# Kernel optimization log

Hardware: AMD Instinct MI355X
Metric: run time of the kernel (lower is better)

Reference implementation:

```python
import jax, jax.numpy as jnp
import numpy as np

TEMPERATURE = 0.5

def setup_inputs() -> dict:
    key = jax.random.key(0)
    k1, k2 = jax.random.split(key)
    B, D = 4096, 256
    return {
        "first_transformed": jax.random.normal(k1, (B, D), dtype=jnp.float32),
        "second_transformed": jax.random.normal(k2, (B, D), dtype=jnp.float32),
    }

def reference(first_transformed, second_transformed):
    B = first_transformed.shape[0]
    z = jnp.concatenate([first_transformed, second_transformed], axis=0)  # [2B, D]
    z = z / jnp.linalg.norm(z, axis=1, keepdims=True)
    sim = jnp.matmul(z, z.T) / TEMPERATURE  # [2B, 2B]
    n = 2 * B
    # exclude self-similarity from the denominator (mask diagonal)
    diag_mask = jnp.eye(n, dtype=bool)
    denom = jax.nn.logsumexp(jnp.where(diag_mask, -jnp.inf, sim), axis=1)  # [2B]
    # positive pair for row i is row (i+B) mod 2B
    pos_idx = (jnp.arange(n) + B) % n
    pos = sim[jnp.arange(n), pos_idx]  # [2B]
    # loss = 1/(2B) * sum_i (-log(exp(pos_i)/denom_i)) = mean(denom - pos)
    return jnp.mean(denom - pos)
```

## Files before the change

kernel.cpp:

```cpp
#include <hip/hip_runtime.h>
#include <hip/hip_bf16.h>
#include <math.h>


#define NROWS 8192
#define BHALF 4096
#define DDIM  256
#define ROWB  512
#define JSPLIT 16
#define JCHUNK (NROWS / JSPLIT)
#define JT 64
#define NTILES (JCHUNK / JT)
#define TILEB (JT * ROWB)

#define SQRT_K1 1.6986436f
#define LN2F 0.6931471805599453f

typedef __attribute__((ext_vector_type(8))) __bf16 bf16x8;
typedef __attribute__((ext_vector_type(4))) float f32x4;

#if __has_builtin(__builtin_amdgcn_exp2f)
#define FEXP2(x) __builtin_amdgcn_exp2f(x)
#else
#define FEXP2(x) __exp2f(x)
#endif
#if __has_builtin(__builtin_amdgcn_logf)
#define FLOG2(x) __builtin_amdgcn_logf(x)
#else
#define FLOG2(x) __log2f(x)
#endif

__device__ __forceinline__ float bfu(unsigned short u) {
  union { unsigned v; float f; } x; x.v = ((unsigned)u) << 16; return x.f;
}

__global__ __launch_bounds__(256) void norm_kernel(
    const float* __restrict__ a, const float* __restrict__ b,
    char* __restrict__ zb, float* __restrict__ selfdot) {
  int row = blockIdx.x * 4 + (threadIdx.x >> 6);
  int lane = threadIdx.x & 63;
  const float* src = (row < BHALF) ? (a + (size_t)row * DDIM)
                                   : (b + (size_t)(row - BHALF) * DDIM);
  float4 v = ((const float4*)src)[lane];
  float ss = v.x * v.x + v.y * v.y + v.z * v.z + v.w * v.w;
  #pragma unroll
  for (int m = 1; m < 64; m <<= 1) ss += __shfl_xor(ss, m, 64);
  float inv = rsqrtf(ss);
  inv = inv * (1.5f - 0.5f * ss * inv * inv);
  float sc = inv * SQRT_K1;

  union { __hip_bfloat16 h; unsigned short u; } c0, c1, c2, c3;
  c0.h = __float2bfloat16(v.x * sc);
  c1.h = __float2bfloat16(v.y * sc);
  c2.h = __float2bfloat16(v.z * sc);
  c3.h = __float2bfloat16(v.w * sc);
  float q0 = bfu(c0.u), q1 = bfu(c1.u), q2 = bfu(c2.u), q3 = bfu(c3.u);
  float sq = q0 * q0 + q1 * q1 + q2 * q2 + q3 * q3;
  #pragma unroll
  for (int m = 1; m < 64; m <<= 1) sq += __shfl_xor(sq, m, 64);

  ushort4 o = make_ushort4(c0.u, c1.u, c2.u, c3.u);
  int off = row * ROWB + ((lane * 8) ^ ((row & 7) << 4));
  *(ushort4*)(zb + off) = o;
  if (lane == 0) selfdot[row] = sq;
}

__global__ __launch_bounds__(256, 2) void sim_kernel(
    const char* __restrict__ zb, float* __restrict__ s_part) {
  __shared__ __align__(16) char lds[2 * TILEB];
  int rb = blockIdx.x;
  int js = blockIdx.y;
  int wave = threadIdx.x >> 6;
  int lane = threadIdx.x & 63;
  int lrow = lane & 15;
  int kgrp = lane >> 4;
  int r0 = rb * 256 + wave * 64;
  int jbase = js * JCHUNK;

  bf16x8 af[4][8];
  {
    int sw = (lrow & 7) << 4;
    #pragma unroll
    for (int rf = 0; rf < 4; ++rf) {
      const char* rp = zb + (size_t)(r0 + rf * 16 + lrow) * ROWB;
      #pragma unroll
      for (int kk = 0; kk < 8; ++kk)
        af[rf][kk] = *(const bf16x8*)(rp + ((kk * 64 + kgrp * 16) ^ sw));
    }
  }

  float sacc[4][4] = {};
  f32x4 C0, C1, C2, C3;
  bf16x8 bfv[8];

  #define STAGE_SLOT(dstbuf, j0, kkh) do {                                    \
    const char* g_ = zb +                                                     \
        (size_t)((j0) + wave * 16 + lrow) * ROWB +                            \
        (((kkh) * 64 + kgrp * 16) ^ ((lane & 7) << 4));                       \
    char* l_ = lds + (dstbuf) * TILEB + (wave * 8 + (kkh)) * 1024;            \
    __builtin_amdgcn_global_load_lds(                                         \
        (const __attribute__((address_space(1))) void*)g_,                    \
        (__attribute__((address_space(3))) void*)l_, 16, 0, 0);               \
  } while (0)

  #define DSREAD(ct) do {                                                     \
    const char* lbr = lds + buf * TILEB + lane * 16;                          \
    _Pragma("unroll")                                                         \
    for (int kk = 0; kk < 8; ++kk)                                            \
      bfv[kk] = *(const bf16x8*)(lbr + ((ct) * 8 + kk) * 1024);               \
  } while (0)

  #define MFMA32() do {                                                       \
    C0 = (f32x4){0.f, 0.f, 0.f, 0.f};                                         \
    C1 = (f32x4){0.f, 0.f, 0.f, 0.f};                                         \
    C2 = (f32x4){0.f, 0.f, 0.f, 0.f};                                         \
    C3 = (f32x4){0.f, 0.f, 0.f, 0.f};                                         \
    __builtin_amdgcn_s_setprio(1);                                            \
    _Pragma("unroll")                                                         \
    for (int kk = 0; kk < 8; ++kk) {                                          \
      C0 = __builtin_amdgcn_mfma_f32_16x16x32_bf16(af[0][kk], bfv[kk], C0, 0, 0, 0); \
      C1 = __builtin_amdgcn_mfma_f32_16x16x32_bf16(af[1][kk], bfv[kk], C1, 0, 0, 0); \
      C2 = __builtin_amdgcn_mfma_f32_16x16x32_bf16(af[2][kk], bfv[kk], C2, 0, 0, 0); \
      C3 = __builtin_amdgcn_mfma_f32_16x16x32_bf16(af[3][kk], bfv[kk], C3, 0, 0, 0); \
    }                                                                         \
    __builtin_amdgcn_s_setprio(0);                                            \
  } while (0)

  #define FLUSHC() do {                                                       \
    _Pragma("unroll")                                                         \
    for (int r = 0; r < 4; ++r) {                                             \
      sacc[0][r] += FEXP2(C0[r]);                                             \
      sacc[1][r] += FEXP2(C1[r]);                                             \
      sacc[2][r] += FEXP2(C2[r]);                                             \
      sacc[3][r] += FEXP2(C3[r]);                                             \
    }                                                                         \
  } while (0)

  #pragma unroll
  for (int kk = 0; kk < 8; ++kk) STAGE_SLOT(0, jbase, kk);
  asm volatile("s_waitcnt vmcnt(0)" ::: "memory");
  __builtin_amdgcn_sched_barrier(0);
  __builtin_amdgcn_s_barrier();

  int buf = 0;
  for (int t = 0; t < NTILES; ++t) {
    bool st = (t + 1 < NTILES);
    int nj = jbase + (t + 1) * JT;
    #pragma unroll
    for (int ct = 0; ct < 4; ++ct) {
      DSREAD(ct);
      if (st) {
        STAGE_SLOT(buf ^ 1, nj, 2 * ct);
        STAGE_SLOT(buf ^ 1, nj, 2 * ct + 1);
      }
      MFMA32();
      FLUSHC();
    }
    if (st) {
      asm volatile("s_waitcnt vmcnt(0)" ::: "memory");
      __builtin_amdgcn_sched_barrier(0);
      __builtin_amdgcn_s_barrier();
    }
    buf ^= 1;
  }
  #undef FLUSHC
  #undef MFMA32
  #undef DSREAD
  #undef STAGE_SLOT

  #pragma unroll
  for (int rf = 0; rf < 4; ++rf) {
    #pragma unroll
    for (int r = 0; r < 4; ++r) {
      float v = sacc[rf][r];
      #pragma unroll
      for (int m = 1; m < 16; m <<= 1) v += __shfl_xor(v, m, 64);
      if (lrow == 0) {
        int grow = r0 + rf * 16 + kgrp * 4 + r;
        s_part[(size_t)grow * JSPLIT + js] = v;
      }
    }
  }
}

__global__ __launch_bounds__(256) void rowterm_kernel(
    const char* __restrict__ zb, const float* __restrict__ s_part,
    const float* __restrict__ selfdot, float* __restrict__ bpart) {
  int wave = threadIdx.x >> 6;
  int lane = threadIdx.x & 63;
  int rbase = blockIdx.x * 16 + wave * 4;
  float wacc = 0.f;
  #pragma unroll
  for (int rr = 0; rr < 4; ++rr) {
    int i = rbase + rr;
    int j = i ^ BHALF;
    int wo = (lane * 8) ^ ((i & 7) << 4);
    ushort4 zi = *(const ushort4*)(zb + (size_t)i * ROWB + wo);
    ushort4 zj = *(const ushort4*)(zb + (size_t)j * ROWB + wo);
    float dot = bfu(zi.x) * bfu(zj.x) + bfu(zi.y) * bfu(zj.y) +
                bfu(zi.z) * bfu(zj.z) + bfu(zi.w) * bfu(zj.w);
    float sp = (lane < JSPLIT) ? s_part[(size_t)i * JSPLIT + lane] : 0.f;
    #pragma unroll
    for (int m = 1; m < 64; m <<= 1) {
      dot += __shfl_xor(dot, m, 64);
      sp += __shfl_xor(sp, m, 64);
    }
    float S = sp - FEXP2(selfdot[i]);
    wacc += LN2F * (FLOG2(S) - dot);
  }
  __shared__ float red[4];
  if (lane == 0) red[wave] = wacc;
  __syncthreads();
  if (threadIdx.x == 0)
    bpart[blockIdx.x] = red[0] + red[1] + red[2] + red[3];
}

__global__ __launch_bounds__(512) void final_kernel(
    const float* __restrict__ bpart, float* __restrict__ out) {
  int t = threadIdx.x;
  float v = bpart[t];
  #pragma unroll
  for (int m = 1; m < 64; m <<= 1) v += __shfl_xor(v, m, 64);
  __shared__ float r2[8];
  if ((t & 63) == 0) r2[t >> 6] = v;
  __syncthreads();
  if (t == 0) {
    float s = 0.f;
    #pragma unroll
    for (int w = 0; w < 8; ++w) s += r2[w];
    out[0] = s / (float)NROWS;
  }
}

extern "C" void kernel_launch(void* const* d_in, const int* in_sizes, int n_in,
                              void* d_out, int out_size, void* d_ws, size_t ws_size,
                              hipStream_t stream) {
  const float* a = (const float*)d_in[0];
  const float* b = (const float*)d_in[1];
  float* out = (float*)d_out;
  char* ws = (char*)d_ws;

  char* zb = ws;
  float* selfdot = (float*)(ws + (size_t)NROWS * ROWB);
  float* s_part = selfdot + NROWS;
  float* bpart = s_part + (size_t)NROWS * JSPLIT;

  hipLaunchKernelGGL(norm_kernel, dim3(NROWS / 4), dim3(256), 0, stream,
                     a, b, zb, selfdot);
  hipLaunchKernelGGL(sim_kernel, dim3(NROWS / 256, JSPLIT), dim3(256), 0,
                     stream, zb, s_part);
  hipLaunchKernelGGL(rowterm_kernel, dim3(512), dim3(256), 0, stream,
                     zb, s_part, selfdot, bpart);
  hipLaunchKernelGGL(final_kernel, dim3(1), dim3(512), 0, stream, bpart, out);
}
```

Before: 47.79 us.

## Exploit symmetry of similarity matrix to compute only upper-triangle tiles

The similarity matrix is symmetric, so each block now computes a 256-row strip against a set of column tiles covering roughly half the matrix, and also accumulates column sums of the exponentials. Those sums are reduced through LDS and written as partial row sums for the transposed rows. The grid becomes a 1D launch of 512 blocks, split into heavy (5 tiles) and light (4 tiles) blocks, and the partial-sum buffer grows to 35 slots per row. This roughly halves MFMA and exp work, at the cost of extra cross-lane and LDS reductions, a barrier every tile, and uneven block lengths.

```diff
diff --git a/kernel.cpp b/kernel.cpp
--- a/kernel.cpp
+++ b/kernel.cpp
@@ -7,11 +7,10 @@
 #define BHALF 4096
 #define DDIM  256
 #define ROWB  512
-#define JSPLIT 16
-#define JCHUNK (NROWS / JSPLIT)
-#define JT 64
-#define NTILES (JCHUNK / JT)
+#define JT    64
 #define TILEB (JT * ROWB)
+#define NSLOT 35
+#define SSTRIDE 40
 
 #define SQRT_K1 1.6986436f
 #define LN2F 0.6931471805599453f
@@ -68,14 +67,21 @@
 __global__ __launch_bounds__(256, 2) void sim_kernel(
     const char* __restrict__ zb, float* __restrict__ s_part) {
   __shared__ __align__(16) char lds[2 * TILEB];
-  int rb = blockIdx.x;
-  int js = blockIdx.y;
+  __shared__ float cred[2][4][64];
+
+  int bid = blockIdx.x;
+  bool heavy = (bid < 128);
+  int t  = heavy ? (bid & 31) : ((bid - 128) & 31);
+  int gg = heavy ? (bid >> 5) : (4 + ((bid - 128) >> 5));
+  int NJT = heavy ? 5 : 4;
+  int ustrip = (t + gg) & 31;
+  int u16 = (t + 16) & 31;
+
   int wave = threadIdx.x >> 6;
   int lane = threadIdx.x & 63;
   int lrow = lane & 15;
   int kgrp = lane >> 4;
-  int r0 = rb * 256 + wave * 64;
-  int jbase = js * JCHUNK;
+  int r0 = t * 256 + wave * 64;
 
   bf16x8 af[4][8];
   {
@@ -90,6 +96,7 @@
   }
 
   float sacc[4][4] = {};
+  float cacc[4] = {};
   f32x4 C0, C1, C2, C3;
   bf16x8 bfv[8];
 
@@ -103,8 +110,8 @@
         (__attribute__((address_space(3))) void*)l_, 16, 0, 0);               \
   } while (0)
 
-  #define DSREAD(ct) do {                                                     \
-    const char* lbr = lds + buf * TILEB + lane * 16;                          \
+  #define DSREAD(bufi, ct) do {                                               \
+    const char* lbr = lds + (bufi) * TILEB + lane * 16;                       \
     _Pragma("unroll")                                                         \
     for (int kk = 0; kk < 8; ++kk)                                            \
       bfv[kk] = *(const bf16x8*)(lbr + ((ct) * 8 + kk) * 1024);               \
@@ -126,61 +133,88 @@
     __builtin_amdgcn_s_setprio(0);                                            \
   } while (0)
 
-  #define FLUSHC() do {                                                       \
+  #define FLUSHC(ct) do {                                                     \
+    float cs = 0.f;                                                           \
     _Pragma("unroll")                                                         \
     for (int r = 0; r < 4; ++r) {                                             \
-      sacc[0][r] += FEXP2(C0[r]);                                             \
-      sacc[1][r] += FEXP2(C1[r]);                                             \
-      sacc[2][r] += FEXP2(C2[r]);                                             \
-      sacc[3][r] += FEXP2(C3[r]);                                             \
+      float e0 = FEXP2(C0[r]), e1 = FEXP2(C1[r]);                             \
+      float e2 = FEXP2(C2[r]), e3 = FEXP2(C3[r]);                             \
+      sacc[0][r] += e0; sacc[1][r] += e1;                                     \
+      sacc[2][r] += e2; sacc[3][r] += e3;                                     \
+      cs += (e0 + e1) + (e2 + e3);                                            \
     }                                                                         \
-  } while (0)
-
-  #pragma unroll
-  for (int kk = 0; kk < 8; ++kk) STAGE_SLOT(0, jbase, kk);
+    cacc[ct] += cs;                                                           \
+  } while (0)
+
+  #pragma unroll
+  for (int kk = 0; kk < 8; ++kk) STAGE_SLOT(0, ustrip * 256, kk);
   asm volatile("s_waitcnt vmcnt(0)" ::: "memory");
   __builtin_amdgcn_sched_barrier(0);
   __builtin_amdgcn_s_barrier();
 
-  int buf = 0;
-  for (int t = 0; t < NTILES; ++t) {
-    bool st = (t + 1 < NTILES);
-    int nj = jbase + (t + 1) * JT;
+  for (int jt = 0; jt < NJT; ++jt) {
+    int nb = jt & 1;
+    bool last = (jt == NJT - 1);
+    int nj = jt + 1;
+    int nextbase = (nj < 4) ? (ustrip * 256 + nj * 64) : (u16 * 256 + gg * 64);
+
     #pragma unroll
     for (int ct = 0; ct < 4; ++ct) {
-      DSREAD(ct);
-      if (st) {
-        STAGE_SLOT(buf ^ 1, nj, 2 * ct);
-        STAGE_SLOT(buf ^ 1, nj, 2 * ct + 1);
+      DSREAD(nb, ct);
+      if (!last) {
+        STAGE_SLOT(nb ^ 1, nextbase, 2 * ct);
+        STAGE_SLOT(nb ^ 1, nextbase, 2 * ct + 1);
       }
       MFMA32();
-      FLUSHC();
-    }
-    if (st) {
-      asm volatile("s_waitcnt vmcnt(0)" ::: "memory");
-      __builtin_amdgcn_sched_barrier(0);
-      __builtin_amdgcn_s_barrier();
-    }
-    buf ^= 1;
+      FLUSHC(ct);
+    }
+
+    bool harvest = (jt < 4) && (gg > 0);
+    if (harvest) {
+      #pragma unroll
+      for (int c2 = 0; c2 < 4; ++c2) {
+        float v = cacc[c2];
+        v += __shfl_xor(v, 16, 64);
+        v += __shfl_xor(v, 32, 64);
+        if (kgrp == 0) cred[jt & 1][wave][c2 * 16 + lrow] = v;
+      }
+    }
+    #pragma unroll
+    for (int c2 = 0; c2 < 4; ++c2) cacc[c2] = 0.f;
+
+    if (jt == 3 || jt == 4) {
+      int slot = (jt == 3) ? gg : 16 + gg;
+      #pragma unroll
+      for (int rf = 0; rf < 4; ++rf) {
+        #pragma unroll
+        for (int r = 0; r < 4; ++r) {
+          float v = sacc[rf][r];
+          #pragma unroll
+          for (int m = 1; m < 16; m <<= 1) v += __shfl_xor(v, m, 64);
+          if (lrow == 0) {
+            int grow = r0 + rf * 16 + kgrp * 4 + r;
+            s_part[(size_t)grow * SSTRIDE + slot] = v;
+          }
+          sacc[rf][r] = 0.f;
+        }
+      }
+    }
+
+    asm volatile("s_waitcnt vmcnt(0)" ::: "memory");
+    __builtin_amdgcn_sched_barrier(0);
+    __builtin_amdgcn_s_barrier();
+
+    if (harvest && wave == (jt & 3)) {
+      int colrow = ustrip * 256 + jt * 64 + lane;
+      float v = cred[jt & 1][0][lane] + cred[jt & 1][1][lane] +
+                cred[jt & 1][2][lane] + cred[jt & 1][3][lane];
+      s_part[(size_t)colrow * SSTRIDE + 19 + gg] = v;
+    }
   }
   #undef FLUSHC
   #undef MFMA32
   #undef DSREAD
   #undef STAGE_SLOT
-
-  #pragma unroll
-  for (int rf = 0; rf < 4; ++rf) {
-    #pragma unroll
-    for (int r = 0; r < 4; ++r) {
-      float v = sacc[rf][r];
-      #pragma unroll
-      for (int m = 1; m < 16; m <<= 1) v += __shfl_xor(v, m, 64);
-      if (lrow == 0) {
-        int grow = r0 + rf * 16 + kgrp * 4 + r;
-        s_part[(size_t)grow * JSPLIT + js] = v;
-      }
-    }
-  }
 }
 
 __global__ __launch_bounds__(256) void rowterm_kernel(
@@ -199,7 +233,7 @@
     ushort4 zj = *(const ushort4*)(zb + (size_t)j * ROWB + wo);
     float dot = bfu(zi.x) * bfu(zj.x) + bfu(zi.y) * bfu(zj.y) +
                 bfu(zi.z) * bfu(zj.z) + bfu(zi.w) * bfu(zj.w);
-    float sp = (lane < JSPLIT) ? s_part[(size_t)i * JSPLIT + lane] : 0.f;
+    float sp = (lane < NSLOT) ? s_part[(size_t)i * SSTRIDE + lane] : 0.f;
     #pragma unroll
     for (int m = 1; m < 64; m <<= 1) {
       dot += __shfl_xor(dot, m, 64);
@@ -243,12 +277,12 @@
   char* zb = ws;
   float* selfdot = (float*)(ws + (size_t)NROWS * ROWB);
   float* s_part = selfdot + NROWS;
-  float* bpart = s_part + (size_t)NROWS * JSPLIT;
+  float* bpart = s_part + (size_t)NROWS * SSTRIDE;
 
   hipLaunchKernelGGL(norm_kernel, dim3(NROWS / 4), dim3(256), 0, stream,
                      a, b, zb, selfdot);
-  hipLaunchKernelGGL(sim_kernel, dim3(NROWS / 256, JSPLIT), dim3(256), 0,
-                     stream, zb, s_part);
+  hipLaunchKernelGGL(sim_kernel, dim3(512), dim3(256), 0, stream,
+                     zb, s_part);
   hipLaunchKernelGGL(rowterm_kernel, dim3(512), dim3(256), 0, stream,
                      zb, s_part, selfdot, bpart);
   hipLaunchKernelGGL(final_kernel, dim3(1), dim3(512), 0, stream, bpart, out);
```

New measurement: 43.59 us. -8.8%, faster.
